# Performance work log

Hardware: AMD Instinct MI355X
Metric: run time of the kernel (lower is better)

Reference implementation:

```python
import jax, jax.numpy as jnp
import numpy as np

NL = 8  # number of wavenet cells


def _causal_dil_conv(x, w, b, dil):
    # x: (B, Cin, T), w: (Cout, Cin, K) -> (B, Cout, T), left-padded (causal)
    pad = (w.shape[-1] - 1) * dil
    y = jax.lax.conv_general_dilated(
        x, w, window_strides=(1,), padding=[(pad, 0)],
        rhs_dilation=(dil,), dimension_numbers=('NCH', 'OIH', 'NCH'))
    return y + b[None, :, None]


def setup_inputs() -> dict:
    key = jax.random.key(0)
    ks = jax.random.split(key, 12)
    T, B, d_lag, d_cov, d, K = 2048, 16, 1, 7, 256, 2
    s = 0.05
    return {
        'x_lag': jax.random.normal(ks[0], (T, B, d_lag), jnp.float32),
        'x_cov': jax.random.normal(ks[1], (T, B, d_cov), jnp.float32),
        'up_W': jax.random.normal(ks[2], (d_lag + d_cov, d), jnp.float32) * s,
        'up_b': jax.random.normal(ks[3], (d,), jnp.float32) * s,
        'dil_w': jax.random.normal(ks[4], (NL, 2 * d, d, K), jnp.float32) * s,
        'dil_b': jax.random.normal(ks[5], (NL, 2 * d), jnp.float32) * s,
        'skip_w': jax.random.normal(ks[6], (NL, 2 * d, d, 1), jnp.float32) * s,
        'skip_b': jax.random.normal(ks[7], (NL, 2 * d), jnp.float32) * s,
        'loc_W': jax.random.normal(ks[8], (d, 1), jnp.float32) * s,
        'loc_b': jax.random.normal(ks[9], (1,), jnp.float32) * s,
        'proj_W': jax.random.normal(ks[10], (1, 1), jnp.float32) * s,
        'proj_b': jax.random.normal(ks[11], (1,), jnp.float32) * s,
        'd_outputseqlen': 96,
    }


def reference(x_lag, x_cov, up_W, up_b, dil_w, dil_b, skip_w, skip_b,
              loc_W, loc_b, proj_W, proj_b, d_outputseqlen):
    T = x_lag.shape[0]
    h = jnp.concatenate([x_lag, x_cov[:T]], axis=-1)          # (T,B,d_lag+d_cov)
    h = h @ up_W + up_b                                        # (T,B,d)
    h = jnp.transpose(h, (1, 2, 0))                            # (B,d,T)
    skip = jnp.zeros_like(h)
    for i in range(NL):
        z = _causal_dil_conv(h, dil_w[i], dil_b[i], 2 ** i)    # (B,2d,T)
        f, g = jnp.split(z, 2, axis=1)
        gated = jnp.tanh(f) * jax.nn.sigmoid(g)                # (B,d,T)
        z2 = _causal_dil_conv(gated, skip_w[i], skip_b[i], 1)  # (B,2d,T)
        h_next, skip_next = jnp.split(z2, 2, axis=1)
        h = h + h_next
        skip = skip + skip_next
    out = jnp.transpose(skip[:, :, -d_outputseqlen:], (2, 0, 1))  # (L,B,d)
    loc = out @ loc_W + loc_b                                     # (L,B,1)
    y = jnp.transpose(loc, (1, 0, 2))[..., None]                  # (B,L,1,1)
    return y @ proj_W + proj_b                                    # (B,L,1,c_out)
```

## Files before the change

kernel.cpp:

```cpp
#include <hip/hip_runtime.h>
#include <math.h>
#include <stdint.h>

#define T_TOTAL 2048
#define NB 16
#define D 256
#define T0 1696
#define TBUF 352
#define TSKIP 1952
#define LOUT 96

typedef __bf16 bf16x8 __attribute__((ext_vector_type(8)));
typedef __bf16 bf16x4v __attribute__((ext_vector_type(4)));
typedef float f32x4 __attribute__((ext_vector_type(4)));

__device__ __forceinline__ void gload_lds16(const void* src, void* lds_dst) {
    auto g = (const __attribute__((address_space(1))) void*)(uintptr_t)src;
    auto l = (__attribute__((address_space(3))) void*)(uintptr_t)(
                 (uint32_t)(uintptr_t)lds_dst);
    __builtin_amdgcn_global_load_lds(g, l, 16, 0, 0);
}

__device__ __forceinline__ void decode_tile(int id, int gridx, int& rt, int& ct) {
    int k = id & 7;
    int j = id >> 3;
    int rpx = gridx >> 6;
    rt = k * rpx + (j >> 3);
    ct = j & 7;
}

__global__ __launch_bounds__(256) void prep_up(
    const float* __restrict__ dil_w, const float* __restrict__ skip_w,
    const float* __restrict__ x_lag, const float* __restrict__ x_cov,
    const float* __restrict__ up_W, const float* __restrict__ up_b,
    const float* __restrict__ loc_W,
    __bf16* __restrict__ wT, __bf16* __restrict__ w2, __bf16* __restrict__ w2T,
    float* __restrict__ hf, __bf16* __restrict__ hb,
    float* __restrict__ vWp)
{
    const int g0 = blockIdx.x * 256 + threadIdx.x;
    const int NT = 2048 * 256;

    for (int u = g0; u < 8 * 512 * 32; u += NT) {
        int j = u & 31;
        int cog = u >> 5;
        const float* src = dil_w + ((size_t)cog << 9) + (j << 4);
        float4 a = *(const float4*)(src);
        float4 b = *(const float4*)(src + 4);
        float4 c = *(const float4*)(src + 8);
        float4 d = *(const float4*)(src + 12);
        bf16x8 t0 = {(__bf16)a.x, (__bf16)a.z, (__bf16)b.x, (__bf16)b.z,
                     (__bf16)c.x, (__bf16)c.z, (__bf16)d.x, (__bf16)d.z};
        bf16x8 t1 = {(__bf16)a.y, (__bf16)a.w, (__bf16)b.y, (__bf16)b.w,
                     (__bf16)c.y, (__bf16)c.w, (__bf16)d.y, (__bf16)d.w};
        *(bf16x8*)(wT + ((size_t)cog << 9) + (j << 3)) = t0;
        *(bf16x8*)(wT + ((size_t)cog << 9) + 256 + (j << 3)) = t1;
    }
    for (int u = g0; u < 7 * 256 * 32; u += NT) {
        int row = u >> 5, j = u & 31;
        int ly = row >> 8, co = row & 255;
        const float* src = skip_w + (((size_t)(ly << 9) + co) << 8) + (j << 3);
        float4 a = *(const float4*)(src);
        float4 b = *(const float4*)(src + 4);
        bf16x8 v = {(__bf16)a.x, (__bf16)a.y, (__bf16)a.z, (__bf16)a.w,
                    (__bf16)b.x, (__bf16)b.y, (__bf16)b.z, (__bf16)b.w};
        *(bf16x8*)(w2 + ((size_t)row << 8) + (j << 3)) = v;
        __bf16* wt = w2T + ((size_t)ly << 16) + (j << 3) * 256 + co;
        #pragma unroll
        for (int e = 0; e < 8; ++e) wt[e << 8] = v[e];
    }
    for (int u = g0; u < TBUF * NB * D; u += NT) {
        int row = u >> 8, c = u & 255;
        int tt = row >> 4, b = row & 15, t = T0 + tt;
        float acc = up_b[c] + x_lag[t * NB + b] * up_W[c];
        const float* cov = &x_cov[(t * NB + b) * 7];
        #pragma unroll
        for (int j = 0; j < 7; ++j)
            acc += cov[j] * up_W[(j + 1) * D + c];
        hf[u] = acc;
        hb[u] = (__bf16)acc;
    }
    for (int u = g0; u < 16384; u += NT) {
        int part = u >> 11;
        int r = u & 2047;
        int ly = r >> 8, ci = r & 255;
        const float* sw = skip_w + (((size_t)(ly << 9) + 256 + (part << 5)) << 8) + ci;
        float acc = 0.f;
        #pragma unroll 8
        for (int c = 0; c < 32; ++c)
            acc += sw[(size_t)c << 8] * loc_W[(part << 5) + c];
        vWp[u] = acc;
    }
}

__global__ __launch_bounds__(512, 4) void prep_v(
    const __bf16* __restrict__ wT, const __bf16* __restrict__ w2T,
    const float* __restrict__ dil_b, const float* __restrict__ skip_b,
    __bf16* __restrict__ V, float* __restrict__ cbias)
{
    __shared__ __align__(16) unsigned char lds[24576];
    const int id = blockIdx.x;
    const int tid = threadIdx.x;
    const int lane = tid & 63, wid = tid >> 6;
    if (id >= 896) {
        int n = (id - 896) * 8 + wid;
        int i1 = n >> 9, n0 = n & 511;
        const __bf16* wrow = wT + (((size_t)(i1 + 1) << 18) + ((size_t)n0 << 9));
        const float* sb = skip_b + (i1 << 9);
        float s = 0.f;
        #pragma unroll
        for (int e = 0; e < 8; ++e) {
            int k = (lane << 3) + e;
            s += sb[k & 255] * (float)wrow[k];
        }
        #pragma unroll
        for (int off = 32; off; off >>= 1) s += __shfl_down(s, off);
        if (lane == 0)
            cbias[(i1 << 9) + n0] = dil_b[((i1 + 1) << 9) + n0] + s;
        return;
    }
    const int i1 = id / 128;
    const int r = id - i1 * 128;
    const int a = r >> 6;
    const int rt = (r & 63) >> 3, ct = r & 7;
    const int n0t = rt << 6;
    const int cb = ct << 5;
    const __bf16* Awt = wT + (((size_t)(i1 + 1) << 18)) + (a << 8);
    const __bf16* Bw = w2T + ((size_t)i1 << 16);
    const int wm = wid >> 1, wn = wid & 1;
    const int l15 = lane & 15, l4 = lane >> 4;
    const int arow = (wid << 3) + (lane >> 3);
    const int ach = lane & 7;
    const int aswz = (ach ^ (arow & 7)) << 3;
    const int brow = (wid << 3) + (lane >> 3);
    const int bswz = (ach ^ (brow & 7)) << 3;

    f32x4 acc = {};
    auto stage = [&](int t, int buf) {
        const int k0 = t << 6;
        unsigned char* base = lds + buf * 12288;
        gload_lds16(Awt + (size_t)(n0t + arow) * 512 + k0 + aswz,
                    base + (wid << 10));
        if (wid < 4)
            gload_lds16(Bw + (size_t)(cb + brow) * 256 + k0 + bswz,
                        base + 8192 + (wid << 10));
    };
    stage(0, 0);
    for (int t = 0; t < 4; ++t) {
        const int buf = t & 1;
        if (t < 3) {
            stage(t + 1, buf ^ 1);
            if (wid < 4) { asm volatile("s_waitcnt vmcnt(2)" ::: "memory"); }
            else         { asm volatile("s_waitcnt vmcnt(1)" ::: "memory"); }
        } else {
            asm volatile("s_waitcnt vmcnt(0)" ::: "memory");
        }
        __builtin_amdgcn_s_barrier();
        const unsigned char* base = lds + buf * 12288;
        #pragma unroll
        for (int ks = 0; ks < 2; ++ks) {
            const int kb = (ks << 6) + (l4 << 4);
            int rr = (wm << 4) + l15;
            bf16x8 av = *(const bf16x8*)(base + rr * 128 + (kb ^ ((rr & 7) << 4)));
            int nn = (wn << 4) + l15;
            int o = nn * 128 + (kb ^ ((nn & 7) << 4));
            bf16x8 bv = *(const bf16x8*)(base + 8192 + o);
            acc = __builtin_amdgcn_mfma_f32_16x16x32_bf16(av, bv, acc, 0, 0, 0);
        }
        __builtin_amdgcn_s_barrier();
    }
    {
        int c = cb + (wn << 4) + l15;
        #pragma unroll
        for (int rr = 0; rr < 4; ++rr) {
            int n = n0t + (wm << 4) + (l4 << 2) + rr;
            V[((size_t)i1 << 18) + (size_t)n * 512 + (a << 8) + c] = (__bf16)acc[rr];
        }
    }
}

__global__ __launch_bounds__(512, 4) void gate_n32(
    const __bf16* __restrict__ hb, __bf16* __restrict__ gated,
    const __bf16* __restrict__ wTl, const float* __restrict__ gbias,
    int tb, int dil, int M)
{
    __shared__ __align__(16) unsigned char lds[32768];
    int rt, ct;
    decode_tile(blockIdx.x, gridDim.x, rt, ct);
    const int m0 = rt << 6;
    if (m0 >= M) return;
    const int cb = ct << 5;
    const int tid = threadIdx.x;
    const int lane = tid & 63, wid = tid >> 6;
    const int wm = wid >> 1, wn = wid & 1;
    const int l15 = lane & 15, l4 = lane >> 4;
    const int arow = (wid << 3) + (lane >> 3);
    const int ach = lane & 7;
    const int aswz = (ach ^ (arow & 7)) << 3;
    const int bwid = wid & 3, bhalf = wid >> 2;
    const int brow = (bwid << 3) + (lane >> 3);
    const int bswz = (ach ^ (brow & 7)) << 3;
    const int roff1 = (tb - T0) * 16;
    const int roff0 = roff1 - dil * 16;

    f32x4 accf = {}, accg = {};
    auto stage = [&](int t, int buf) {
        const int k0 = t << 6;
        const int ci0 = k0 & 255;
        const int roff = (t < 4) ? roff0 : roff1;
        unsigned char* base = lds + buf * 16384;
        int m = m0 + arow; if (m >= M) m = M - 1;
        gload_lds16(hb + (size_t)(m + roff) * 256 + ci0 + aswz,
                    base + (wid << 10));
        gload_lds16(wTl + (size_t)(cb + bhalf * 256 + brow) * 512 + k0 + bswz,
                    base + 8192 + (bhalf << 12) + (bwid << 10));
    };
    stage(0, 0);
    for (int t = 0; t < 8; ++t) {
        const int buf = t & 1;
        if (t < 7) {
            stage(t + 1, buf ^ 1);
            asm volatile("s_waitcnt vmcnt(2)" ::: "memory");
        } else {
            asm volatile("s_waitcnt vmcnt(0)" ::: "memory");
        }
        __builtin_amdgcn_s_barrier();
        const unsigned char* base = lds + buf * 16384;
        __builtin_amdgcn_s_setprio(1);
        #pragma unroll
        for (int ks = 0; ks < 2; ++ks) {
            const int kb = (ks << 6) + (l4 << 4);
            int r = (wm << 4) + l15;
            bf16x8 av = *(const bf16x8*)(base + r * 128 + (kb ^ ((r & 7) << 4)));
            int n = (wn << 4) + l15;
            int o = n * 128 + (kb ^ ((n & 7) << 4));
            bf16x8 bfv = *(const bf16x8*)(base + 8192 + o);
            bf16x8 bgv = *(const bf16x8*)(base + 12288 + o);
            accf = __builtin_amdgcn_mfma_f32_16x16x32_bf16(av, bfv, accf, 0, 0, 0);
            accg = __builtin_amdgcn_mfma_f32_16x16x32_bf16(av, bgv, accg, 0, 0, 0);
        }
        __builtin_amdgcn_s_setprio(0);
        __builtin_amdgcn_s_barrier();
    }
    {
        int c = cb + (wn << 4) + l15;
        float bfb = gbias[c], bgb = gbias[c + 256];
        #pragma unroll
        for (int r = 0; r < 4; ++r) {
            int m = m0 + (wm << 4) + (l4 << 2) + r;
            if (m < M) {
                float fv = accf[r] + bfb;
                float gv = accg[r] + bgb;
                float th = 2.0f / (1.0f + __expf(-2.0f * fv)) - 1.0f;
                float sg = 1.0f / (1.0f + __expf(-gv));
                gated[(size_t)m * 256 + c] = (__bf16)(th * sg);
            }
        }
    }
}

__global__ __launch_bounds__(512, 4) void fused_layer(
    const __bf16* __restrict__ hb_r, const __bf16* __restrict__ gb_r,
    __bf16* __restrict__ gb_w,
    const __bf16* __restrict__ wTl, const __bf16* __restrict__ Vl,
    const float* __restrict__ cbias_l,
    int tb_g, int dil_g, int Mg, int ngate,
    const __bf16* __restrict__ w2l, const float* __restrict__ sbias,
    float* __restrict__ hf, __bf16* __restrict__ hb_w,
    int tb_s, int Ms, int nskip,
    const float* __restrict__ vWl, float* __restrict__ accb,
    int goff_t, int first_tail)
{
    __shared__ __align__(16) unsigned char lds[32768];
    const int id = blockIdx.x;
    const int tid = threadIdx.x;
    const int lane = tid & 63, wid = tid >> 6;
    const int wm = wid >> 1, wn = wid & 1;
    const int l15 = lane & 15, l4 = lane >> 4;
    const int ach = lane & 7;

    if (id < ngate) {
        int rt, ct;
        decode_tile(id, ngate, rt, ct);
        const int m0 = rt << 6;
        if (m0 >= Mg) return;
        const int cb = ct << 5;
        const int arow = (wid << 3) + (lane >> 3);
        const int aswz = (ach ^ (arow & 7)) << 3;
        const int bwid = wid & 3, bhalf = wid >> 2;
        const int brow = (bwid << 3) + (lane >> 3);
        const int bswz = (ach ^ (brow & 7)) << 3;
        const int roff1 = (tb_g - T0) * 16;
        const int roff0 = roff1 - dil_g * 16;
        const int goff1 = dil_g * 16;

        f32x4 accf = {}, accg = {};
        auto stage = [&](int t, int buf) {
            const int k0 = t << 6;
            unsigned char* base = lds + buf * 16384;
            int m = m0 + arow; if (m >= Mg) m = Mg - 1;
            if (t < 8) {
                const int ci0 = k0 & 255;
                const int roff = (t < 4) ? roff0 : roff1;
                gload_lds16(hb_r + (size_t)(m + roff) * 256 + ci0 + aswz,
                            base + (wid << 10));
                gload_lds16(wTl + (size_t)(cb + bhalf * 256 + brow) * 512 + k0 + bswz,
                            base + 8192 + (bhalf << 12) + (bwid << 10));
            } else {
                const int c0 = k0 & 255;
                const int go = (t < 12) ? 0 : goff1;
                gload_lds16(gb_r + (size_t)(m + go) * 256 + c0 + aswz,
                            base + (wid << 10));
                gload_lds16(Vl + (size_t)(cb + bhalf * 256 + brow) * 512 + (k0 - 512) + bswz,
                            base + 8192 + (bhalf << 12) + (bwid << 10));
            }
        };
        stage(0, 0);
        for (int t = 0; t < 16; ++t) {
            const int buf = t & 1;
            if (t < 15) {
                stage(t + 1, buf ^ 1);
                asm volatile("s_waitcnt vmcnt(2)" ::: "memory");
            } else {
                asm volatile("s_waitcnt vmcnt(0)" ::: "memory");
            }
            __builtin_amdgcn_s_barrier();
            const unsigned char* base = lds + buf * 16384;
            __builtin_amdgcn_s_setprio(1);
            #pragma unroll
            for (int ks = 0; ks < 2; ++ks) {
                const int kb = (ks << 6) + (l4 << 4);
                int r = (wm << 4) + l15;
                bf16x8 av = *(const bf16x8*)(base + r * 128 + (kb ^ ((r & 7) << 4)));
                int n = (wn << 4) + l15;
                int o = n * 128 + (kb ^ ((n & 7) << 4));
                bf16x8 bfv = *(const bf16x8*)(base + 8192 + o);
                bf16x8 bgv = *(const bf16x8*)(base + 12288 + o);
                accf = __builtin_amdgcn_mfma_f32_16x16x32_bf16(av, bfv, accf, 0, 0, 0);
                accg = __builtin_amdgcn_mfma_f32_16x16x32_bf16(av, bgv, accg, 0, 0, 0);
            }
            __builtin_amdgcn_s_setprio(0);
            __builtin_amdgcn_s_barrier();
        }
        {
            int c = cb + (wn << 4) + l15;
            float bfb = cbias_l[c], bgb = cbias_l[c + 256];
            #pragma unroll
            for (int r = 0; r < 4; ++r) {
                int m = m0 + (wm << 4) + (l4 << 2) + r;
                if (m < Mg) {
                    float fv = accf[r] + bfb;
                    float gv = accg[r] + bgb;
                    float th = 2.0f / (1.0f + __expf(-2.0f * fv)) - 1.0f;
                    float sg = 1.0f / (1.0f + __expf(-gv));
                    gb_w[(size_t)m * 256 + c] = (__bf16)(th * sg);
                }
            }
        }
    } else if (id < ngate + nskip) {
        int rt, ct;
        decode_tile(id - ngate, nskip, rt, ct);
        const int m0 = rt << 6;
        if (m0 >= Ms) return;
        const int cb = ct << 5;
        const int arow = (wid << 3) + (lane >> 3);
        const int aswz = (ach ^ (arow & 7)) << 3;
        const int brow = (wid << 3) + (lane >> 3);
        const int bswz = (ach ^ (brow & 7)) << 3;
        const int roff1 = (tb_s - T0) * 16;

        f32x4 acch = {};
        auto stage = [&](int t, int buf) {
            const int k0 = t << 6;
            unsigned char* base = lds + buf * 12288;
            int m = m0 + arow; if (m >= Ms) m = Ms - 1;
            gload_lds16(gb_r + (size_t)m * 256 + k0 + aswz,
                        base + (wid << 10));
            if (wid < 4)
                gload_lds16(w2l + (size_t)(cb + brow) * 256 + k0 + bswz,
                            base + 8192 + (wid << 10));
        };
        stage(0, 0);
        for (int t = 0; t < 4; ++t) {
            const int buf = t & 1;
            if (t < 3) {
                stage(t + 1, buf ^ 1);
                if (wid < 4) { asm volatile("s_waitcnt vmcnt(2)" ::: "memory"); }
                else         { asm volatile("s_waitcnt vmcnt(1)" ::: "memory"); }
            } else {
                asm volatile("s_waitcnt vmcnt(0)" ::: "memory");
            }
            __builtin_amdgcn_s_barrier();
            const unsigned char* base = lds + buf * 12288;
            __builtin_amdgcn_s_setprio(1);
            #pragma unroll
            for (int ks = 0; ks < 2; ++ks) {
                const int kb = (ks << 6) + (l4 << 4);
                int r = (wm << 4) + l15;
                bf16x8 av = *(const bf16x8*)(base + r * 128 + (kb ^ ((r & 7) << 4)));
                int n = (wn << 4) + l15;
                int o = n * 128 + (kb ^ ((n & 7) << 4));
                bf16x8 bhv = *(const bf16x8*)(base + 8192 + o);
                acch = __builtin_amdgcn_mfma_f32_16x16x32_bf16(av, bhv, acch, 0, 0, 0);
            }
            __builtin_amdgcn_s_setprio(0);
            __builtin_amdgcn_s_barrier();
        }
        {
            int c = cb + (wn << 4) + l15;
            float bhb = sbias[c];
            #pragma unroll
            for (int r = 0; r < 4; ++r) {
                int m = m0 + (wm << 4) + (l4 << 2) + r;
                if (m < Ms) {
                    size_t hi = (size_t)(m + roff1) * 256 + c;
                    float hv = hf[hi] + acch[r] + bhb;
                    hf[hi] = hv;
                    hb_w[hi] = (__bf16)hv;
                }
            }
        }
    } else {
        int o = (id - ngate - nskip) * 8 + wid;
        const __bf16* g = gb_r + (size_t)(o + goff_t) * 256;
        bf16x4v gv = *(const bf16x4v*)(g + (lane << 2));
        float4 vw = {0.f, 0.f, 0.f, 0.f};
        #pragma unroll
        for (int p = 0; p < 8; ++p) {
            float4 vp = *(const float4*)(vWl + (p << 11) + (lane << 2));
            vw.x += vp.x; vw.y += vp.y; vw.z += vp.z; vw.w += vp.w;
        }
        float s = (float)gv[0] * vw.x + (float)gv[1] * vw.y
                + (float)gv[2] * vw.z + (float)gv[3] * vw.w;
        #pragma unroll
        for (int off = 32; off; off >>= 1) s += __shfl_down(s, off);
        if (lane == 0) {
            if (first_tail) accb[o] = s;
            else accb[o] += s;
        }
    }
}

__global__ __launch_bounds__(256) void final_v3(
    const __bf16* __restrict__ gb7, const float* __restrict__ vWp,
    const float* __restrict__ accb, const float* __restrict__ skip_b,
    const float* __restrict__ loc_W, const float* __restrict__ loc_b,
    const float* __restrict__ proj_W, const float* __restrict__ proj_b,
    float* __restrict__ out)
{
    int tid = threadIdx.x;
    int wid = tid >> 6, lane = tid & 63;
    int o = blockIdx.x * 4 + wid;
    bf16x4v gv = *(const bf16x4v*)(gb7 + ((size_t)o << 8) + (lane << 2));
    float4 vw = {0.f, 0.f, 0.f, 0.f};
    #pragma unroll
    for (int p = 0; p < 8; ++p) {
        float4 vp = *(const float4*)(vWp + (p << 11) + (7 << 8) + (lane << 2));
        vw.x += vp.x; vw.y += vp.y; vw.z += vp.z; vw.w += vp.w;
    }
    float acc = (float)gv[0] * vw.x + (float)gv[1] * vw.y
              + (float)gv[2] * vw.z + (float)gv[3] * vw.w;
    #pragma unroll
    for (int j = 0; j < 32; ++j) {
        int idx = lane + (j << 6);
        int ly = idx >> 8, c = idx & 255;
        acc += skip_b[(ly << 9) + 256 + c] * loc_W[c];
    }
    #pragma unroll
    for (int off = 32; off; off >>= 1) acc += __shfl_down(acc, off);
    if (lane == 0) {
        int l = o >> 4, b = o & 15;
        out[b * LOUT + l] = (acc + accb[o] + loc_b[0]) * proj_W[0] + proj_b[0];
    }
}

extern "C" void kernel_launch(void* const* d_in, const int* in_sizes, int n_in,
                              void* d_out, int out_size, void* d_ws, size_t ws_size,
                              hipStream_t stream)
{
    const float* x_lag  = (const float*)d_in[0];
    const float* x_cov  = (const float*)d_in[1];
    const float* up_W   = (const float*)d_in[2];
    const float* up_b   = (const float*)d_in[3];
    const float* dil_w  = (const float*)d_in[4];
    const float* dil_b  = (const float*)d_in[5];
    const float* skip_w = (const float*)d_in[6];
    const float* skip_b = (const float*)d_in[7];
    const float* loc_W  = (const float*)d_in[8];
    const float* loc_b  = (const float*)d_in[9];
    const float* proj_W = (const float*)d_in[10];
    const float* proj_b = (const float*)d_in[11];
    float* out = (float*)d_out;

    unsigned char* ws = (unsigned char*)d_ws;
    float*  hf    = (float*)ws;
    __bf16* hbuf[2] = { (__bf16*)(ws + 5767168),
                        (__bf16*)(ws + 8650752) };
    __bf16* gbuf[2] = { (__bf16*)(ws + 11534336),
                        (__bf16*)(ws + 14417920) };
    __bf16* wT    = (__bf16*)(ws + 17301504);
    __bf16* V     = (__bf16*)(ws + 21495808);
    __bf16* w2    = (__bf16*)(ws + 25165824);
    __bf16* w2T   = (__bf16*)(ws + 26083328);
    float*  vWp   = (float*)(ws + 27000832);
    float*  cbias = (float*)(ws + 27066368);
    float*  accb  = (float*)(ws + 27080704);

    hipLaunchKernelGGL(prep_up, dim3(2048), dim3(256), 0, stream,
                       dil_w, skip_w, x_lag, x_cov, up_W, up_b, loc_W,
                       wT, w2, w2T, hf, hbuf[0], vWp);
    hipLaunchKernelGGL(prep_v, dim3(1344), dim3(512), 0, stream,
                       wT, w2T, dil_b, skip_b, V, cbias);

    {
        int tb = T0 + 2, M = (T_TOTAL - tb) * NB;
        int mtp = (((M + 63) >> 6) + 7) & ~7;
        hipLaunchKernelGGL(gate_n32, dim3(mtp * 8), dim3(512), 0, stream,
                           hbuf[0], gbuf[0], wT, dil_b, tb, 1, M);
    }
    for (int i = 1; i < 8; ++i) {
        int dil = 1 << i;
        int tb_g = T0 + 2 * dil;
        int Mg = (T_TOTAL - tb_g) * NB;
        int ngate = ((((Mg + 63) >> 6) + 7) & ~7) * 8;
        int s = i - 1;
        int tb_s = T0 + 2 * (1 << s);
        int Ms = (T_TOTAL - tb_s) * NB;
        int nskip = (i < 7) ? ((((Ms + 63) >> 6) + 7) & ~7) * 8 : 0;
        hipLaunchKernelGGL(fused_layer, dim3(ngate + nskip + 192), dim3(512), 0,
                           stream,
                           hbuf[s & 1], gbuf[s & 1], gbuf[i & 1],
                           wT + ((size_t)i << 18), V + ((size_t)s << 18),
                           cbias + (s << 9),
                           tb_g, dil, Mg, ngate,
                           w2 + ((size_t)s << 16), skip_b + (s << 9),
                           hf, hbuf[i & 1], tb_s, Ms, nskip,
                           vWp + (s << 8), accb,
                           (TSKIP - tb_s) * 16, i == 1 ? 1 : 0);
    }
    hipLaunchKernelGGL(final_v3, dim3(LOUT * NB / 4), dim3(256), 0, stream,
                       gbuf[1], vWp, accb, skip_b, loc_W, loc_b, proj_W, proj_b,
                       out);
}
```

Measured before the change: 127.8 us.

## Restructure layer schedule: separate gate/skip kernels early, substitute skip weights only for last layers

Replaces the per-layer fused gate+skip kernel, which folded the previous layer's skip GEMM into the next gate via precomputed V matrices for all layers, with separate gate and skip_h launches for layers 0-4. The V substitution is kept only for layers 6 and 7, computed inside a new d0_kernel that also runs layer 0's gate. Gated outputs of the tail timesteps are saved and the final reduction sums all eight layers directly instead of using an accumulated skip buffer. The aim is to cut precompute work and the longer K dimension of the fused GEMMs, at the cost of more kernel launches and an extra hf/hb round trip per early layer.

```diff
diff --git a/kernel.cpp b/kernel.cpp
--- a/kernel.cpp
+++ b/kernel.cpp
@@ -21,10 +21,10 @@
     __builtin_amdgcn_global_load_lds(g, l, 16, 0, 0);
 }
 
-__device__ __forceinline__ void decode_tile(int id, int gridx, int& rt, int& ct) {
+__device__ __forceinline__ void decode_tile(int id, int ngate, int& rt, int& ct) {
     int k = id & 7;
     int j = id >> 3;
-    int rpx = gridx >> 6;
+    int rpx = ngate >> 6;
     rt = k * rpx + (j >> 3);
     ct = j & 7;
 }
@@ -56,7 +56,7 @@
         *(bf16x8*)(wT + ((size_t)cog << 9) + (j << 3)) = t0;
         *(bf16x8*)(wT + ((size_t)cog << 9) + 256 + (j << 3)) = t1;
     }
-    for (int u = g0; u < 7 * 256 * 32; u += NT) {
+    for (int u = g0; u < 5 * 256 * 32; u += NT) {
         int row = u >> 5, j = u & 31;
         int ly = row >> 8, co = row & 255;
         const float* src = skip_w + (((size_t)(ly << 9) + co) << 8) + (j << 3);
@@ -65,9 +65,18 @@
         bf16x8 v = {(__bf16)a.x, (__bf16)a.y, (__bf16)a.z, (__bf16)a.w,
                     (__bf16)b.x, (__bf16)b.y, (__bf16)b.z, (__bf16)b.w};
         *(bf16x8*)(w2 + ((size_t)row << 8) + (j << 3)) = v;
-        __bf16* wt = w2T + ((size_t)ly << 16) + (j << 3) * 256 + co;
-        #pragma unroll
-        for (int e = 0; e < 8; ++e) wt[e << 8] = v[e];
+    }
+    for (int u = g0; u < 2 * 256 * 32; u += NT) {
+        int row = u >> 5, j = u & 31;
+        int lyr = row >> 8, co = row & 255;
+        int ly = 5 + lyr;
+        const float* src = skip_w + (((size_t)(ly << 9) + co) << 8) + (j << 3);
+        float4 a = *(const float4*)(src);
+        float4 b = *(const float4*)(src + 4);
+        float v[8] = {a.x, a.y, a.z, a.w, b.x, b.y, b.z, b.w};
+        __bf16* wt = w2T + ((size_t)lyr << 16) + ((size_t)(j << 3) << 8) + co;
+        #pragma unroll
+        for (int e = 0; e < 8; ++e) wt[(size_t)e << 8] = (__bf16)v[e];
     }
     for (int u = g0; u < TBUF * NB * D; u += NT) {
         int row = u >> 8, c = u & 255;
@@ -93,95 +102,177 @@
     }
 }
 
-__global__ __launch_bounds__(512, 4) void prep_v(
-    const __bf16* __restrict__ wT, const __bf16* __restrict__ w2T,
-    const float* __restrict__ dil_b, const float* __restrict__ skip_b,
-    __bf16* __restrict__ V, float* __restrict__ cbias)
+__global__ __launch_bounds__(512, 4) void d0_kernel(
+    const __bf16* __restrict__ hb, __bf16* __restrict__ gated,
+    const __bf16* __restrict__ wT, const float* __restrict__ dil_b,
+    const __bf16* __restrict__ w2T, const float* __restrict__ skip_b,
+    __bf16* __restrict__ V, float* __restrict__ cbias,
+    __bf16* __restrict__ gsv, int ngate, int tb, int M)
 {
-    __shared__ __align__(16) unsigned char lds[24576];
+    __shared__ __align__(16) unsigned char lds[32768];
     const int id = blockIdx.x;
     const int tid = threadIdx.x;
     const int lane = tid & 63, wid = tid >> 6;
-    if (id >= 896) {
-        int n = (id - 896) * 8 + wid;
-        int i1 = n >> 9, n0 = n & 511;
-        const __bf16* wrow = wT + (((size_t)(i1 + 1) << 18) + ((size_t)n0 << 9));
-        const float* sb = skip_b + (i1 << 9);
+    const int wm = wid >> 1, wn = wid & 1;
+    const int l15 = lane & 15, l4 = lane >> 4;
+    const int ach = lane & 7;
+
+    if (id < ngate) {
+        int rt, ct;
+        decode_tile(id, ngate, rt, ct);
+        const int m0 = rt << 6;
+        if (m0 >= M) return;
+        const int cb = ct << 5;
+        const int arow = (wid << 3) + (lane >> 3);
+        const int aswz = (ach ^ (arow & 7)) << 3;
+        const int bwid = wid & 3, bhalf = wid >> 2;
+        const int brow = (bwid << 3) + (lane >> 3);
+        const int bswz = (ach ^ (brow & 7)) << 3;
+        const int roff1 = (tb - T0) * 16;
+        const int roff0 = roff1 - 16;
+
+        f32x4 accf = {}, accg = {};
+        auto stage = [&](int t, int buf) {
+            const int k0 = t << 6;
+            const int ci0 = k0 & 255;
+            const int roff = (t < 4) ? roff0 : roff1;
+            unsigned char* base = lds + buf * 16384;
+            int m = m0 + arow; if (m >= M) m = M - 1;
+            gload_lds16(hb + (size_t)(m + roff) * 256 + ci0 + aswz,
+                        base + (wid << 10));
+            gload_lds16(wT + (size_t)(cb + bhalf * 256 + brow) * 512 + k0 + bswz,
+                        base + 8192 + (bhalf << 12) + (bwid << 10));
+        };
+        stage(0, 0);
+        for (int t = 0; t < 8; ++t) {
+            const int buf = t & 1;
+            if (t < 7) {
+                stage(t + 1, buf ^ 1);
+                asm volatile("s_waitcnt vmcnt(2)" ::: "memory");
+            } else {
+                asm volatile("s_waitcnt vmcnt(0)" ::: "memory");
+            }
+            __builtin_amdgcn_s_barrier();
+            const unsigned char* base = lds + buf * 16384;
+            __builtin_amdgcn_s_setprio(1);
+            #pragma unroll
+            for (int ks = 0; ks < 2; ++ks) {
+                const int kb = (ks << 6) + (l4 << 4);
+                int r = (wm << 4) + l15;
+                bf16x8 av = *(const bf16x8*)(base + r * 128 + (kb ^ ((r & 7) << 4)));
+                int n = (wn << 4) + l15;
+                int o = n * 128 + (kb ^ ((n & 7) << 4));
+                bf16x8 bfv = *(const bf16x8*)(base + 8192 + o);
+                bf16x8 bgv = *(const bf16x8*)(base + 12288 + o);
+                accf = __builtin_amdgcn_mfma_f32_16x16x32_bf16(av, bfv, accf, 0, 0, 0);
+                accg = __builtin_amdgcn_mfma_f32_16x16x32_bf16(av, bgv, accg, 0, 0, 0);
+            }
+            __builtin_amdgcn_s_setprio(0);
+            __builtin_amdgcn_s_barrier();
+        }
+        {
+            const int ms0 = (TSKIP - tb) * 16;
+            const int soff = (tb - TSKIP) * 16;
+            int c = cb + (wn << 4) + l15;
+            float bfb = dil_b[c], bgb = dil_b[c + 256];
+            #pragma unroll
+            for (int r = 0; r < 4; ++r) {
+                int m = m0 + (wm << 4) + (l4 << 2) + r;
+                if (m < M) {
+                    float fv = accf[r] + bfb;
+                    float gv = accg[r] + bgb;
+                    float th = 2.0f / (1.0f + __expf(-2.0f * fv)) - 1.0f;
+                    float sg = 1.0f / (1.0f + __expf(-gv));
+                    __bf16 val = (__bf16)(th * sg);
+                    gated[(size_t)m * 256 + c] = val;
+                    if (m >= ms0)
+                        gsv[(size_t)(m + soff) * 256 + c] = val;
+                }
+            }
+        }
+    } else if (id < ngate + 384) {
+        int v = id - ngate;
+        int pair = v >> 7;
+        int r = v & 127;
+        int tgt = (pair == 0) ? 6 : 7;
+        int srcix = (pair == 2) ? 1 : 0;
+        int a = r >> 6;
+        int rt = (r & 63) >> 3, ct = r & 7;
+        const int n0t = rt << 6;
+        const int cb = ct << 5;
+        const __bf16* Awt = wT + ((size_t)tgt << 18) + (a << 8);
+        const __bf16* Bw = w2T + ((size_t)srcix << 16);
+        const int arow = (wid << 3) + (lane >> 3);
+        const int aswz = (ach ^ (arow & 7)) << 3;
+        const int brow = (wid << 3) + (lane >> 3);
+        const int bswz = (ach ^ (brow & 7)) << 3;
+
+        f32x4 acc = {};
+        auto stage = [&](int t, int buf) {
+            const int k0 = t << 6;
+            unsigned char* base = lds + buf * 12288;
+            gload_lds16(Awt + (size_t)(n0t + arow) * 512 + k0 + aswz,
+                        base + (wid << 10));
+            if (wid < 4)
+                gload_lds16(Bw + (size_t)(cb + brow) * 256 + k0 + bswz,
+                            base + 8192 + (wid << 10));
+        };
+        stage(0, 0);
+        for (int t = 0; t < 4; ++t) {
+            const int buf = t & 1;
+            if (t < 3) {
+                stage(t + 1, buf ^ 1);
+                if (wid < 4) { asm volatile("s_waitcnt vmcnt(2)" ::: "memory"); }
+                else         { asm volatile("s_waitcnt vmcnt(1)" ::: "memory"); }
+            } else {
+                asm volatile("s_waitcnt vmcnt(0)" ::: "memory");
+            }
+            __builtin_amdgcn_s_barrier();
+            const unsigned char* base = lds + buf * 12288;
+            #pragma unroll
+            for (int ks = 0; ks < 2; ++ks) {
+                const int kb = (ks << 6) + (l4 << 4);
+                int rr = (wm << 4) + l15;
+                bf16x8 av = *(const bf16x8*)(base + rr * 128 + (kb ^ ((rr & 7) << 4)));
+                int nn = (wn << 4) + l15;
+                int o = nn * 128 + (kb ^ ((nn & 7) << 4));
+                bf16x8 bv = *(const bf16x8*)(base + 8192 + o);
+                acc = __builtin_amdgcn_mfma_f32_16x16x32_bf16(av, bv, acc, 0, 0, 0);
+            }
+            __builtin_amdgcn_s_barrier();
+        }
+        {
+            int c = cb + (wn << 4) + l15;
+            #pragma unroll
+            for (int rr = 0; rr < 4; ++rr) {
+                int n = n0t + (wm << 4) + (l4 << 2) + rr;
+                V[((size_t)pair << 18) + (size_t)n * 512 + (a << 8) + c] = (__bf16)acc[rr];
+            }
+        }
+    } else {
+        int cblk = id - ngate - 384;
+        int n = cblk * 8 + wid;
+        int tl = n >> 9, n0 = n & 511;
+        const __bf16* wrow = wT + ((size_t)(6 + tl) << 18) + ((size_t)n0 << 9);
         float s = 0.f;
         #pragma unroll
         for (int e = 0; e < 8; ++e) {
             int k = (lane << 3) + e;
-            s += sb[k & 255] * (float)wrow[k];
+            float sbv = skip_b[(5 << 9) + (k & 255)];
+            if (tl == 1) sbv += skip_b[(6 << 9) + (k & 255)];
+            s += sbv * (float)wrow[k];
         }
         #pragma unroll
         for (int off = 32; off; off >>= 1) s += __shfl_down(s, off);
         if (lane == 0)
-            cbias[(i1 << 9) + n0] = dil_b[((i1 + 1) << 9) + n0] + s;
-        return;
-    }
-    const int i1 = id / 128;
-    const int r = id - i1 * 128;
-    const int a = r >> 6;
-    const int rt = (r & 63) >> 3, ct = r & 7;
-    const int n0t = rt << 6;
-    const int cb = ct << 5;
-    const __bf16* Awt = wT + (((size_t)(i1 + 1) << 18)) + (a << 8);
-    const __bf16* Bw = w2T + ((size_t)i1 << 16);
-    const int wm = wid >> 1, wn = wid & 1;
-    const int l15 = lane & 15, l4 = lane >> 4;
-    const int arow = (wid << 3) + (lane >> 3);
-    const int ach = lane & 7;
-    const int aswz = (ach ^ (arow & 7)) << 3;
-    const int brow = (wid << 3) + (lane >> 3);
-    const int bswz = (ach ^ (brow & 7)) << 3;
-
-    f32x4 acc = {};
-    auto stage = [&](int t, int buf) {
-        const int k0 = t << 6;
-        unsigned char* base = lds + buf * 12288;
-        gload_lds16(Awt + (size_t)(n0t + arow) * 512 + k0 + aswz,
-                    base + (wid << 10));
-        if (wid < 4)
-            gload_lds16(Bw + (size_t)(cb + brow) * 256 + k0 + bswz,
-                        base + 8192 + (wid << 10));
-    };
-    stage(0, 0);
-    for (int t = 0; t < 4; ++t) {
-        const int buf = t & 1;
-        if (t < 3) {
-            stage(t + 1, buf ^ 1);
-            if (wid < 4) { asm volatile("s_waitcnt vmcnt(2)" ::: "memory"); }
-            else         { asm volatile("s_waitcnt vmcnt(1)" ::: "memory"); }
-        } else {
-            asm volatile("s_waitcnt vmcnt(0)" ::: "memory");
-        }
-        __builtin_amdgcn_s_barrier();
-        const unsigned char* base = lds + buf * 12288;
-        #pragma unroll
-        for (int ks = 0; ks < 2; ++ks) {
-            const int kb = (ks << 6) + (l4 << 4);
-            int rr = (wm << 4) + l15;
-            bf16x8 av = *(const bf16x8*)(base + rr * 128 + (kb ^ ((rr & 7) << 4)));
-            int nn = (wn << 4) + l15;
-            int o = nn * 128 + (kb ^ ((nn & 7) << 4));
-            bf16x8 bv = *(const bf16x8*)(base + 8192 + o);
-            acc = __builtin_amdgcn_mfma_f32_16x16x32_bf16(av, bv, acc, 0, 0, 0);
-        }
-        __builtin_amdgcn_s_barrier();
-    }
-    {
-        int c = cb + (wn << 4) + l15;
-        #pragma unroll
-        for (int rr = 0; rr < 4; ++rr) {
-            int n = n0t + (wm << 4) + (l4 << 2) + rr;
-            V[((size_t)i1 << 18) + (size_t)n * 512 + (a << 8) + c] = (__bf16)acc[rr];
-        }
+            cbias[(tl << 9) + n0] = dil_b[((6 + tl) << 9) + n0] + s;
     }
 }
 
 __global__ __launch_bounds__(512, 4) void gate_n32(
-    const __bf16* __restrict__ hb, __bf16* __restrict__ gated,
+    const __bf16* __restrict__ hb, __bf16* __restrict__ gout,
     const __bf16* __restrict__ wTl, const float* __restrict__ gbias,
+    __bf16* __restrict__ gsv, int do_save,
     int tb, int dil, int M)
 {
     __shared__ __align__(16) unsigned char lds[32768];
@@ -243,6 +334,8 @@
         __builtin_amdgcn_s_barrier();
     }
     {
+        const int ms0 = (TSKIP - tb) * 16;
+        const int soff = (tb - TSKIP) * 16;
         int c = cb + (wn << 4) + l15;
         float bfb = gbias[c], bgb = gbias[c + 256];
         #pragma unroll
@@ -253,197 +346,188 @@
                 float gv = accg[r] + bgb;
                 float th = 2.0f / (1.0f + __expf(-2.0f * fv)) - 1.0f;
                 float sg = 1.0f / (1.0f + __expf(-gv));
-                gated[(size_t)m * 256 + c] = (__bf16)(th * sg);
-            }
-        }
-    }
-}
-
-__global__ __launch_bounds__(512, 4) void fused_layer(
-    const __bf16* __restrict__ hb_r, const __bf16* __restrict__ gb_r,
-    __bf16* __restrict__ gb_w,
-    const __bf16* __restrict__ wTl, const __bf16* __restrict__ Vl,
-    const float* __restrict__ cbias_l,
-    int tb_g, int dil_g, int Mg, int ngate,
-    const __bf16* __restrict__ w2l, const float* __restrict__ sbias,
-    float* __restrict__ hf, __bf16* __restrict__ hb_w,
-    int tb_s, int Ms, int nskip,
-    const float* __restrict__ vWl, float* __restrict__ accb,
-    int goff_t, int first_tail)
+                __bf16 val = (__bf16)(th * sg);
+                gout[(size_t)m * 256 + c] = val;
+                if (do_save && m >= ms0)
+                    gsv[(size_t)(m + soff) * 256 + c] = val;
+            }
+        }
+    }
+}
+
+__global__ __launch_bounds__(512, 4) void gate_sub(
+    const __bf16* __restrict__ hb,
+    const __bf16* __restrict__ g1, const __bf16* __restrict__ g2,
+    __bf16* __restrict__ gout,
+    const __bf16* __restrict__ Bh, const __bf16* __restrict__ Bv1,
+    const __bf16* __restrict__ Bv2, const float* __restrict__ cbias_l,
+    int tb, int dil, int M, int nsteps,
+    int hro0, int hro1, int g1o0, int g1o1, int g2o0, int g2o1)
 {
     __shared__ __align__(16) unsigned char lds[32768];
-    const int id = blockIdx.x;
+    int rt, ct;
+    decode_tile(blockIdx.x, gridDim.x, rt, ct);
+    const int m0 = rt << 6;
+    if (m0 >= M) return;
+    const int cb = ct << 5;
     const int tid = threadIdx.x;
     const int lane = tid & 63, wid = tid >> 6;
     const int wm = wid >> 1, wn = wid & 1;
     const int l15 = lane & 15, l4 = lane >> 4;
+    const int arow = (wid << 3) + (lane >> 3);
     const int ach = lane & 7;
-
-    if (id < ngate) {
-        int rt, ct;
-        decode_tile(id, ngate, rt, ct);
-        const int m0 = rt << 6;
-        if (m0 >= Mg) return;
-        const int cb = ct << 5;
-        const int arow = (wid << 3) + (lane >> 3);
-        const int aswz = (ach ^ (arow & 7)) << 3;
-        const int bwid = wid & 3, bhalf = wid >> 2;
-        const int brow = (bwid << 3) + (lane >> 3);
-        const int bswz = (ach ^ (brow & 7)) << 3;
-        const int roff1 = (tb_g - T0) * 16;
-        const int roff0 = roff1 - dil_g * 16;
-        const int goff1 = dil_g * 16;
-
-        f32x4 accf = {}, accg = {};
-        auto stage = [&](int t, int buf) {
-            const int k0 = t << 6;
-            unsigned char* base = lds + buf * 16384;
-            int m = m0 + arow; if (m >= Mg) m = Mg - 1;
-            if (t < 8) {
-                const int ci0 = k0 & 255;
-                const int roff = (t < 4) ? roff0 : roff1;
-                gload_lds16(hb_r + (size_t)(m + roff) * 256 + ci0 + aswz,
-                            base + (wid << 10));
-                gload_lds16(wTl + (size_t)(cb + bhalf * 256 + brow) * 512 + k0 + bswz,
-                            base + 8192 + (bhalf << 12) + (bwid << 10));
-            } else {
-                const int c0 = k0 & 255;
-                const int go = (t < 12) ? 0 : goff1;
-                gload_lds16(gb_r + (size_t)(m + go) * 256 + c0 + aswz,
-                            base + (wid << 10));
-                gload_lds16(Vl + (size_t)(cb + bhalf * 256 + brow) * 512 + (k0 - 512) + bswz,
-                            base + 8192 + (bhalf << 12) + (bwid << 10));
-            }
-        };
-        stage(0, 0);
-        for (int t = 0; t < 16; ++t) {
-            const int buf = t & 1;
-            if (t < 15) {
-                stage(t + 1, buf ^ 1);
-                asm volatile("s_waitcnt vmcnt(2)" ::: "memory");
-            } else {
-                asm volatile("s_waitcnt vmcnt(0)" ::: "memory");
-            }
-            __builtin_amdgcn_s_barrier();
-            const unsigned char* base = lds + buf * 16384;
-            __builtin_amdgcn_s_setprio(1);
-            #pragma unroll
-            for (int ks = 0; ks < 2; ++ks) {
-                const int kb = (ks << 6) + (l4 << 4);
-                int r = (wm << 4) + l15;
-                bf16x8 av = *(const bf16x8*)(base + r * 128 + (kb ^ ((r & 7) << 4)));
-                int n = (wn << 4) + l15;
-                int o = n * 128 + (kb ^ ((n & 7) << 4));
-                bf16x8 bfv = *(const bf16x8*)(base + 8192 + o);
-                bf16x8 bgv = *(const bf16x8*)(base + 12288 + o);
-                accf = __builtin_amdgcn_mfma_f32_16x16x32_bf16(av, bfv, accf, 0, 0, 0);
-                accg = __builtin_amdgcn_mfma_f32_16x16x32_bf16(av, bgv, accg, 0, 0, 0);
-            }
-            __builtin_amdgcn_s_setprio(0);
-            __builtin_amdgcn_s_barrier();
-        }
-        {
-            int c = cb + (wn << 4) + l15;
-            float bfb = cbias_l[c], bgb = cbias_l[c + 256];
-            #pragma unroll
-            for (int r = 0; r < 4; ++r) {
-                int m = m0 + (wm << 4) + (l4 << 2) + r;
-                if (m < Mg) {
-                    float fv = accf[r] + bfb;
-                    float gv = accg[r] + bgb;
-                    float th = 2.0f / (1.0f + __expf(-2.0f * fv)) - 1.0f;
-                    float sg = 1.0f / (1.0f + __expf(-gv));
-                    gb_w[(size_t)m * 256 + c] = (__bf16)(th * sg);
-                }
-            }
-        }
-    } else if (id < ngate + nskip) {
-        int rt, ct;
-        decode_tile(id - ngate, nskip, rt, ct);
-        const int m0 = rt << 6;
-        if (m0 >= Ms) return;
-        const int cb = ct << 5;
-        const int arow = (wid << 3) + (lane >> 3);
-        const int aswz = (ach ^ (arow & 7)) << 3;
-        const int brow = (wid << 3) + (lane >> 3);
-        const int bswz = (ach ^ (brow & 7)) << 3;
-        const int roff1 = (tb_s - T0) * 16;
-
-        f32x4 acch = {};
-        auto stage = [&](int t, int buf) {
-            const int k0 = t << 6;
-            unsigned char* base = lds + buf * 12288;
-            int m = m0 + arow; if (m >= Ms) m = Ms - 1;
-            gload_lds16(gb_r + (size_t)m * 256 + k0 + aswz,
-                        base + (wid << 10));
-            if (wid < 4)
-                gload_lds16(w2l + (size_t)(cb + brow) * 256 + k0 + bswz,
-                            base + 8192 + (wid << 10));
-        };
-        stage(0, 0);
-        for (int t = 0; t < 4; ++t) {
-            const int buf = t & 1;
-            if (t < 3) {
-                stage(t + 1, buf ^ 1);
-                if (wid < 4) { asm volatile("s_waitcnt vmcnt(2)" ::: "memory"); }
-                else         { asm volatile("s_waitcnt vmcnt(1)" ::: "memory"); }
-            } else {
-                asm volatile("s_waitcnt vmcnt(0)" ::: "memory");
-            }
-            __builtin_amdgcn_s_barrier();
-            const unsigned char* base = lds + buf * 12288;
-            __builtin_amdgcn_s_setprio(1);
-            #pragma unroll
-            for (int ks = 0; ks < 2; ++ks) {
-                const int kb = (ks << 6) + (l4 << 4);
-                int r = (wm << 4) + l15;
-                bf16x8 av = *(const bf16x8*)(base + r * 128 + (kb ^ ((r & 7) << 4)));
-                int n = (wn << 4) + l15;
-                int o = n * 128 + (kb ^ ((n & 7) << 4));
-                bf16x8 bhv = *(const bf16x8*)(base + 8192 + o);
-                acch = __builtin_amdgcn_mfma_f32_16x16x32_bf16(av, bhv, acch, 0, 0, 0);
-            }
-            __builtin_amdgcn_s_setprio(0);
-            __builtin_amdgcn_s_barrier();
-        }
-        {
-            int c = cb + (wn << 4) + l15;
-            float bhb = sbias[c];
-            #pragma unroll
-            for (int r = 0; r < 4; ++r) {
-                int m = m0 + (wm << 4) + (l4 << 2) + r;
-                if (m < Ms) {
-                    size_t hi = (size_t)(m + roff1) * 256 + c;
-                    float hv = hf[hi] + acch[r] + bhb;
-                    hf[hi] = hv;
-                    hb_w[hi] = (__bf16)hv;
-                }
-            }
-        }
-    } else {
-        int o = (id - ngate - nskip) * 8 + wid;
-        const __bf16* g = gb_r + (size_t)(o + goff_t) * 256;
-        bf16x4v gv = *(const bf16x4v*)(g + (lane << 2));
-        float4 vw = {0.f, 0.f, 0.f, 0.f};
-        #pragma unroll
-        for (int p = 0; p < 8; ++p) {
-            float4 vp = *(const float4*)(vWl + (p << 11) + (lane << 2));
-            vw.x += vp.x; vw.y += vp.y; vw.z += vp.z; vw.w += vp.w;
-        }
-        float s = (float)gv[0] * vw.x + (float)gv[1] * vw.y
-                + (float)gv[2] * vw.z + (float)gv[3] * vw.w;
-        #pragma unroll
-        for (int off = 32; off; off >>= 1) s += __shfl_down(s, off);
-        if (lane == 0) {
-            if (first_tail) accb[o] = s;
-            else accb[o] += s;
-        }
-    }
-}
-
-__global__ __launch_bounds__(256) void final_v3(
-    const __bf16* __restrict__ gb7, const float* __restrict__ vWp,
-    const float* __restrict__ accb, const float* __restrict__ skip_b,
+    const int aswz = (ach ^ (arow & 7)) << 3;
+    const int bwid = wid & 3, bhalf = wid >> 2;
+    const int brow = (bwid << 3) + (lane >> 3);
+    const int bswz = (ach ^ (brow & 7)) << 3;
+
+    f32x4 accf = {}, accg = {};
+    auto stage = [&](int t, int buf) {
+        unsigned char* base = lds + buf * 16384;
+        int m = m0 + arow; if (m >= M) m = M - 1;
+        const __bf16* asrc;
+        const __bf16* bsrc;
+        int ks;
+        if (t < 8) {
+            ks = t << 6;
+            asrc = hb + (size_t)(m + ((t < 4) ? hro0 : hro1)) * 256 + (ks & 255);
+            bsrc = Bh;
+        } else if (t < 16) {
+            ks = (t - 8) << 6;
+            asrc = g1 + (size_t)(m + ((t < 12) ? g1o0 : g1o1)) * 256 + (ks & 255);
+            bsrc = Bv1;
+        } else {
+            ks = (t - 16) << 6;
+            asrc = g2 + (size_t)(m + ((t < 20) ? g2o0 : g2o1)) * 256 + (ks & 255);
+            bsrc = Bv2;
+        }
+        gload_lds16(asrc + aswz, base + (wid << 10));
+        gload_lds16(bsrc + (size_t)(cb + bhalf * 256 + brow) * 512 + ks + bswz,
+                    base + 8192 + (bhalf << 12) + (bwid << 10));
+    };
+    stage(0, 0);
+    for (int t = 0; t < nsteps; ++t) {
+        const int buf = t & 1;
+        if (t < nsteps - 1) {
+            stage(t + 1, buf ^ 1);
+            asm volatile("s_waitcnt vmcnt(2)" ::: "memory");
+        } else {
+            asm volatile("s_waitcnt vmcnt(0)" ::: "memory");
+        }
+        __builtin_amdgcn_s_barrier();
+        const unsigned char* base = lds + buf * 16384;
+        __builtin_amdgcn_s_setprio(1);
+        #pragma unroll
+        for (int ks = 0; ks < 2; ++ks) {
+            const int kb = (ks << 6) + (l4 << 4);
+            int r = (wm << 4) + l15;
+            bf16x8 av = *(const bf16x8*)(base + r * 128 + (kb ^ ((r & 7) << 4)));
+            int n = (wn << 4) + l15;
+            int o = n * 128 + (kb ^ ((n & 7) << 4));
+            bf16x8 bfv = *(const bf16x8*)(base + 8192 + o);
+            bf16x8 bgv = *(const bf16x8*)(base + 12288 + o);
+            accf = __builtin_amdgcn_mfma_f32_16x16x32_bf16(av, bfv, accf, 0, 0, 0);
+            accg = __builtin_amdgcn_mfma_f32_16x16x32_bf16(av, bgv, accg, 0, 0, 0);
+        }
+        __builtin_amdgcn_s_setprio(0);
+        __builtin_amdgcn_s_barrier();
+    }
+    {
+        int c = cb + (wn << 4) + l15;
+        float bfb = cbias_l[c], bgb = cbias_l[c + 256];
+        #pragma unroll
+        for (int r = 0; r < 4; ++r) {
+            int m = m0 + (wm << 4) + (l4 << 2) + r;
+            if (m < M) {
+                float fv = accf[r] + bfb;
+                float gv = accg[r] + bgb;
+                float th = 2.0f / (1.0f + __expf(-2.0f * fv)) - 1.0f;
+                float sg = 1.0f / (1.0f + __expf(-gv));
+                gout[(size_t)m * 256 + c] = (__bf16)(th * sg);
+            }
+        }
+    }
+}
+
+__global__ __launch_bounds__(512, 4) void skip_h(
+    const __bf16* __restrict__ gated, const __bf16* __restrict__ w2l,
+    float* __restrict__ hf, __bf16* __restrict__ hb,
+    const float* __restrict__ sbias, int tb, int M)
+{
+    __shared__ __align__(16) unsigned char lds[24576];
+    int rt, ct;
+    decode_tile(blockIdx.x, gridDim.x, rt, ct);
+    const int m0 = rt << 6;
+    if (m0 >= M) return;
+    const int cb = ct << 5;
+    const int tid = threadIdx.x;
+    const int lane = tid & 63, wid = tid >> 6;
+    const int wm = wid >> 1, wn = wid & 1;
+    const int l15 = lane & 15, l4 = lane >> 4;
+    const int arow = (wid << 3) + (lane >> 3);
+    const int ach = lane & 7;
+    const int aswz = (ach ^ (arow & 7)) << 3;
+    const int brow = (wid << 3) + (lane >> 3);
+    const int bswz = (ach ^ (brow & 7)) << 3;
+    const int roff1 = (tb - T0) * 16;
+
+    f32x4 acch = {};
+    auto stage = [&](int t, int buf) {
+        const int k0 = t << 6;
+        unsigned char* base = lds + buf * 12288;
+        int m = m0 + arow; if (m >= M) m = M - 1;
+        gload_lds16(gated + (size_t)m * 256 + k0 + aswz,
+                    base + (wid << 10));
+        if (wid < 4)
+            gload_lds16(w2l + (size_t)(cb + brow) * 256 + k0 + bswz,
+                        base + 8192 + (wid << 10));
+    };
+    stage(0, 0);
+    for (int t = 0; t < 4; ++t) {
+        const int buf = t & 1;
+        if (t < 3) {
+            stage(t + 1, buf ^ 1);
+            if (wid < 4) { asm volatile("s_waitcnt vmcnt(2)" ::: "memory"); }
+            else         { asm volatile("s_waitcnt vmcnt(1)" ::: "memory"); }
+        } else {
+            asm volatile("s_waitcnt vmcnt(0)" ::: "memory");
+        }
+        __builtin_amdgcn_s_barrier();
+        const unsigned char* base = lds + buf * 12288;
+        __builtin_amdgcn_s_setprio(1);
+        #pragma unroll
+        for (int ks = 0; ks < 2; ++ks) {
+            const int kb = (ks << 6) + (l4 << 4);
+            int r = (wm << 4) + l15;
+            bf16x8 av = *(const bf16x8*)(base + r * 128 + (kb ^ ((r & 7) << 4)));
+            int n = (wn << 4) + l15;
+            int o = n * 128 + (kb ^ ((n & 7) << 4));
+            bf16x8 bhv = *(const bf16x8*)(base + 8192 + o);
+            acch = __builtin_amdgcn_mfma_f32_16x16x32_bf16(av, bhv, acch, 0, 0, 0);
+        }
+        __builtin_amdgcn_s_setprio(0);
+        __builtin_amdgcn_s_barrier();
+    }
+    {
+        int c = cb + (wn << 4) + l15;
+        float bhb = sbias[c];
+        #pragma unroll
+        for (int r = 0; r < 4; ++r) {
+            int m = m0 + (wm << 4) + (l4 << 2) + r;
+            if (m < M) {
+                size_t hi = (size_t)(m + roff1) * 256 + c;
+                float hv = hf[hi] + acch[r] + bhb;
+                hf[hi] = hv;
+                hb[hi] = (__bf16)hv;
+            }
+        }
+    }
+}
+
+__global__ __launch_bounds__(256) void final_v4(
+    const __bf16* __restrict__ gsave, const __bf16* __restrict__ gA,
+    const __bf16* __restrict__ gB, const __bf16* __restrict__ g7,
+    const float* __restrict__ vWp, const float* __restrict__ skip_b,
     const float* __restrict__ loc_W, const float* __restrict__ loc_b,
     const float* __restrict__ proj_W, const float* __restrict__ proj_b,
     float* __restrict__ out)
@@ -451,15 +535,23 @@
     int tid = threadIdx.x;
     int wid = tid >> 6, lane = tid & 63;
     int o = blockIdx.x * 4 + wid;
-    bf16x4v gv = *(const bf16x4v*)(gb7 + ((size_t)o << 8) + (lane << 2));
-    float4 vw = {0.f, 0.f, 0.f, 0.f};
+    const __bf16* bases[8] = {
+        gsave,                gsave + 1536 * 256,     gsave + 2 * 1536 * 256,
+        gsave + 3 * 1536 * 256, gsave + 4 * 1536 * 256,
+        gA + 3072 * 256,      gB + 2048 * 256,        g7 };
+    float acc = 0.f;
     #pragma unroll
-    for (int p = 0; p < 8; ++p) {
-        float4 vp = *(const float4*)(vWp + (p << 11) + (7 << 8) + (lane << 2));
-        vw.x += vp.x; vw.y += vp.y; vw.z += vp.z; vw.w += vp.w;
-    }
-    float acc = (float)gv[0] * vw.x + (float)gv[1] * vw.y
-              + (float)gv[2] * vw.z + (float)gv[3] * vw.w;
+    for (int ly = 0; ly < 8; ++ly) {
+        bf16x4v gv = *(const bf16x4v*)(bases[ly] + ((size_t)o << 8) + (lane << 2));
+        float4 vw = {0.f, 0.f, 0.f, 0.f};
+        #pragma unroll
+        for (int p = 0; p < 8; ++p) {
+            float4 vp = *(const float4*)(vWp + (p << 11) + (ly << 8) + (lane << 2));
+            vw.x += vp.x; vw.y += vp.y; vw.z += vp.z; vw.w += vp.w;
+        }
+        acc += (float)gv[0] * vw.x + (float)gv[1] * vw.y
+             + (float)gv[2] * vw.z + (float)gv[3] * vw.w;
+    }
     #pragma unroll
     for (int j = 0; j < 32; ++j) {
         int idx = lane + (j << 6);
@@ -470,7 +562,7 @@
     for (int off = 32; off; off >>= 1) acc += __shfl_down(acc, off);
     if (lane == 0) {
         int l = o >> 4, b = o & 15;
-        out[b * LOUT + l] = (acc + accb[o] + loc_b[0]) * proj_W[0] + proj_b[0];
+        out[b * LOUT + l] = (acc + loc_b[0]) * proj_W[0] + proj_b[0];
     }
 }
 
@@ -494,51 +586,72 @@
 
     unsigned char* ws = (unsigned char*)d_ws;
     float*  hf    = (float*)ws;
-    __bf16* hbuf[2] = { (__bf16*)(ws + 5767168),
-                        (__bf16*)(ws + 8650752) };
-    __bf16* gbuf[2] = { (__bf16*)(ws + 11534336),
-                        (__bf16*)(ws + 14417920) };
-    __bf16* wT    = (__bf16*)(ws + 17301504);
-    __bf16* V     = (__bf16*)(ws + 21495808);
-    __bf16* w2    = (__bf16*)(ws + 25165824);
-    __bf16* w2T   = (__bf16*)(ws + 26083328);
-    float*  vWp   = (float*)(ws + 27000832);
-    float*  cbias = (float*)(ws + 27066368);
-    float*  accb  = (float*)(ws + 27080704);
+    __bf16* hb    = (__bf16*)(ws + 5767168);
+    __bf16* gated = (__bf16*)(ws + 8650752);
+    __bf16* gA    = (__bf16*)(ws + 11534336);
+    __bf16* gB    = (__bf16*)(ws + 13893632);
+    __bf16* gsave = (__bf16*)(ws + 15728640);
+    __bf16* wT    = (__bf16*)(ws + 19660800);
+    __bf16* w2    = (__bf16*)(ws + 23855104);
+    __bf16* w2T   = (__bf16*)(ws + 24510464);
+    __bf16* V     = (__bf16*)(ws + 24772608);
+    float*  vWp   = (float*)(ws + 26345472);
+    float*  cbias = (float*)(ws + 26411008);
 
     hipLaunchKernelGGL(prep_up, dim3(2048), dim3(256), 0, stream,
                        dil_w, skip_w, x_lag, x_cov, up_W, up_b, loc_W,
-                       wT, w2, w2T, hf, hbuf[0], vWp);
-    hipLaunchKernelGGL(prep_v, dim3(1344), dim3(512), 0, stream,
-                       wT, w2T, dil_b, skip_b, V, cbias);
+                       wT, w2, w2T, hf, hb, vWp);
 
     {
         int tb = T0 + 2, M = (T_TOTAL - tb) * NB;
         int mtp = (((M + 63) >> 6) + 7) & ~7;
+        int ng0 = mtp * 8;
+        hipLaunchKernelGGL(d0_kernel, dim3(ng0 + 384 + 128), dim3(512), 0, stream,
+                           hb, gated, wT, dil_b, w2T, skip_b, V, cbias,
+                           gsave, ng0, tb, M);
+        hipLaunchKernelGGL(skip_h, dim3(ng0), dim3(512), 0, stream,
+                           gated, w2, hf, hb, skip_b, tb, M);
+    }
+    for (int i = 1; i < 5; ++i) {
+        int dil = 1 << i;
+        int tb = T0 + 2 * dil;
+        int M = (T_TOTAL - tb) * NB;
+        int mtp = (((M + 63) >> 6) + 7) & ~7;
         hipLaunchKernelGGL(gate_n32, dim3(mtp * 8), dim3(512), 0, stream,
-                           hbuf[0], gbuf[0], wT, dil_b, tb, 1, M);
-    }
-    for (int i = 1; i < 8; ++i) {
-        int dil = 1 << i;
-        int tb_g = T0 + 2 * dil;
-        int Mg = (T_TOTAL - tb_g) * NB;
-        int ngate = ((((Mg + 63) >> 6) + 7) & ~7) * 8;
-        int s = i - 1;
-        int tb_s = T0 + 2 * (1 << s);
-        int Ms = (T_TOTAL - tb_s) * NB;
-        int nskip = (i < 7) ? ((((Ms + 63) >> 6) + 7) & ~7) * 8 : 0;
-        hipLaunchKernelGGL(fused_layer, dim3(ngate + nskip + 192), dim3(512), 0,
-                           stream,
-                           hbuf[s & 1], gbuf[s & 1], gbuf[i & 1],
-                           wT + ((size_t)i << 18), V + ((size_t)s << 18),
-                           cbias + (s << 9),
-                           tb_g, dil, Mg, ngate,
-                           w2 + ((size_t)s << 16), skip_b + (s << 9),
-                           hf, hbuf[i & 1], tb_s, Ms, nskip,
-                           vWp + (s << 8), accb,
-                           (TSKIP - tb_s) * 16, i == 1 ? 1 : 0);
-    }
-    hipLaunchKernelGGL(final_v3, dim3(LOUT * NB / 4), dim3(256), 0, stream,
-                       gbuf[1], vWp, accb, skip_b, loc_W, loc_b, proj_W, proj_b,
-                       out);
-}
+                           hb, gated, wT + ((size_t)i << 18),
+                           dil_b + (i << 9),
+                           gsave + (size_t)i * 1536 * 256, 1, tb, dil, M);
+        hipLaunchKernelGGL(skip_h, dim3(mtp * 8), dim3(512), 0, stream,
+                           gated, w2 + ((size_t)i << 16), hf, hb,
+                           skip_b + (i << 9), tb, M);
+    }
+    {
+        int tb = T0 + 64, M = (T_TOTAL - tb) * NB;
+        int mtp = (((M + 63) >> 6) + 7) & ~7;
+        hipLaunchKernelGGL(gate_n32, dim3(mtp * 8), dim3(512), 0, stream,
+                           hb, gA, wT + ((size_t)5 << 18), dil_b + (5 << 9),
+                           gsave, 0, tb, 32, M);
+    }
+    {
+        int tb = T0 + 128, M = (T_TOTAL - tb) * NB;
+        int mtp = (((M + 63) >> 6) + 7) & ~7;
+        hipLaunchKernelGGL(gate_sub, dim3(mtp * 8), dim3(512), 0, stream,
+                           hb, gA, gA, gB,
+                           wT + ((size_t)6 << 18), V, V, cbias,
+                           tb, 64, M, 16,
+                           1024, 2048, 0, 1024, 0, 0);
+    }
+    {
+        int tb = T0 + 256, M = (T_TOTAL - tb) * NB;
+        int mtp = (((M + 63) >> 6) + 7) & ~7;
+        hipLaunchKernelGGL(gate_sub, dim3(mtp * 8), dim3(512), 0, stream,
+                           hb, gA, gB, gated,
+                           wT + ((size_t)7 << 18), V + (1 << 18), V + (2 << 18),
+                           cbias + 512,
+                           tb, 128, M, 24,
+                           2048, 4096, 1024, 3072, 0, 2048);
+    }
+    hipLaunchKernelGGL(final_v4, dim3(LOUT * NB / 4), dim3(256), 0, stream,
+                       gsave, gA, gB, gated, vWp, skip_b,
+                       loc_W, loc_b, proj_W, proj_b, out);
+}
```

After: 124.9 us. -2.3%, faster.
